# Optimization experiments

Hardware: AMD Instinct MI355X
Metric: run time of the kernel (lower is better)

## Reference

```python
import jax, jax.numpy as jnp
import numpy as np

N, E = 50000, 800000
IN_D, HID_D, OUT_D = 128, 128, 64
BN_EPS = 1e-5


def setup_inputs() -> dict:
    key = jax.random.key(0)
    ks = jax.random.split(key, 16)
    x = jax.random.normal(ks[0], (N, IN_D), dtype=jnp.float32)
    edge_index = jax.random.randint(ks[1], (2, E), 0, N, dtype=jnp.int64)
    edge_weight = jax.random.uniform(ks[2], (E,), dtype=jnp.float32)
    s = 0.05  # xavier-ish small gain
    inp = {
        'x': x, 'edge_index': edge_index, 'edge_weight': edge_weight,
        # SAGEConv 1: lin_l (aggregated, with bias), lin_r (root, no bias)
        'W1l': jax.random.normal(ks[3], (HID_D, IN_D), jnp.float32) * s,
        'b1': jnp.zeros((HID_D,), jnp.float32),
        'W1r': jax.random.normal(ks[4], (HID_D, IN_D), jnp.float32) * s,
        # SAGEConv 2
        'W2l': jax.random.normal(ks[5], (HID_D, HID_D), jnp.float32) * s,
        'b2': jnp.zeros((HID_D,), jnp.float32),
        'W2r': jax.random.normal(ks[6], (HID_D, HID_D), jnp.float32) * s,
        # SAGEConv 3
        'W3l': jax.random.normal(ks[7], (OUT_D, HID_D), jnp.float32) * s,
        'b3': jnp.zeros((OUT_D,), jnp.float32),
        'W3r': jax.random.normal(ks[8], (OUT_D, HID_D), jnp.float32) * s,
        # BatchNorm (eval mode: running stats)
        'bn1_g': jnp.ones((HID_D,), jnp.float32),
        'bn1_b': jnp.zeros((HID_D,), jnp.float32),
        'bn1_m': jax.random.normal(ks[9], (HID_D,), jnp.float32) * 0.01,
        'bn1_v': jnp.ones((HID_D,), jnp.float32) + jax.random.uniform(ks[10], (HID_D,), jnp.float32) * 0.1,
        'bn2_g': jnp.ones((HID_D,), jnp.float32),
        'bn2_b': jnp.zeros((HID_D,), jnp.float32),
        'bn2_m': jax.random.normal(ks[11], (HID_D,), jnp.float32) * 0.01,
        'bn2_v': jnp.ones((HID_D,), jnp.float32) + jax.random.uniform(ks[12], (HID_D,), jnp.float32) * 0.1,
    }
    return inp


def _sage_conv(x, src, dst, ew, Wl, bl, Wr):
    # message: x_j * w_ij ; aggregate: mean over incoming edges of node i
    msg = x[src] * ew[:, None]                      # [E, D]
    agg = jax.ops.segment_sum(msg, dst, num_segments=N)
    cnt = jax.ops.segment_sum(jnp.ones_like(ew), dst, num_segments=N)
    mean = agg / jnp.maximum(cnt, 1.0)[:, None]     # [N, D]
    return mean @ Wl.T + bl + x @ Wr.T


def _bn_eval(x, g, b, m, v):
    return (x - m) * (g * jax.lax.rsqrt(v + BN_EPS)) + b


def reference(x, edge_index, edge_weight,
              W1l, b1, W1r, W2l, b2, W2r, W3l, b3, W3r,
              bn1_g, bn1_b, bn1_m, bn1_v, bn2_g, bn2_b, bn2_m, bn2_v):
    src, dst = edge_index[0], edge_index[1]
    h = _sage_conv(x, src, dst, edge_weight, W1l, b1, W1r)
    h = _bn_eval(h, bn1_g, bn1_b, bn1_m, bn1_v)
    h = jnp.where(h >= 0, h, 0.1 * h)  # leaky_relu(0.1); dropout inactive (eval)
    h = _sage_conv(h, src, dst, edge_weight, W2l, b2, W2r)
    h = _bn_eval(h, bn2_g, bn2_b, bn2_m, bn2_v)
    h = jnp.where(h >= 0, h, 0.1 * h)
    h = _sage_conv(h, src, dst, edge_weight, W3l, b3, W3r)
    # F.normalize(p=2, dim=1)
    norm = jnp.maximum(jnp.linalg.norm(h, axis=1, keepdims=True), 1e-12)
    return h / norm
```

## Files before the change

kernel.cpp:

```cpp
#include <hip/hip_runtime.h>
#include <hip/hip_bf16.h>

#define IN_D 128
#define BN_EPS 1e-5f

typedef short bf8 __attribute__((ext_vector_type(8)));
typedef float f32x4 __attribute__((ext_vector_type(4)));

__device__ __forceinline__ ushort f2bf(float f) {
    unsigned u = __float_as_uint(f);
    unsigned r = u + 0x7fffu + ((u >> 16) & 1u);
    return (ushort)(r >> 16);
}


__global__ void k_hist(const int* __restrict__ ei, int* __restrict__ deg, int E, int n) {
    int e = blockIdx.x * 256 + threadIdx.x;
    if (e < E) {
        int dst = ei[E + e];
        if (dst >= 0 && dst < n) atomicAdd(&deg[dst], 1);
    }
}

__global__ void k_block_sum(const int* __restrict__ deg, int* __restrict__ bsum, int n) {
    __shared__ int sdata[256];
    int i = blockIdx.x * 256 + threadIdx.x;
    int v = (i < n) ? deg[i] : 0;
    sdata[threadIdx.x] = v;
    __syncthreads();
    for (int s = 128; s > 0; s >>= 1) {
        if (threadIdx.x < s) sdata[threadIdx.x] += sdata[threadIdx.x + s];
        __syncthreads();
    }
    if (threadIdx.x == 0) bsum[blockIdx.x] = sdata[0];
}

__global__ void k_scan_bsum(int* __restrict__ bsum, int nb) {
    __shared__ int s[256];
    int t = threadIdx.x;
    int v = (t < nb) ? bsum[t] : 0;
    s[t] = v;
    __syncthreads();
    for (int off = 1; off < 256; off <<= 1) {
        int u = (t >= off) ? s[t - off] : 0;
        __syncthreads();
        s[t] += u;
        __syncthreads();
    }
    if (t < nb) bsum[t] = s[t] - v;
}

__global__ void k_scan_deg(const int* __restrict__ deg, const int* __restrict__ boff,
                           int* __restrict__ rowptr, int* __restrict__ cursor,
                           float* __restrict__ invcnt, int n) {
    __shared__ int s[256];
    int t = threadIdx.x;
    int i = blockIdx.x * 256 + t;
    int v = (i < n) ? deg[i] : 0;
    s[t] = v;
    __syncthreads();
    for (int off = 1; off < 256; off <<= 1) {
        int u = (t >= off) ? s[t - off] : 0;
        __syncthreads();
        s[t] += u;
        __syncthreads();
    }
    int incl = s[t];
    int excl = incl - v;
    int base = boff[blockIdx.x];
    if (i < n) {
        rowptr[i] = base + excl;
        cursor[i] = base + excl;
        invcnt[i] = 1.0f / (float)(v < 1 ? 1 : v);
        if (i == n - 1) rowptr[n] = base + incl;
    }
}

__global__ void k_fill(const int* __restrict__ ei, const float* __restrict__ ew,
                       int* __restrict__ cursor, int2* __restrict__ csr, int E, int n) {
    int e = blockIdx.x * 256 + threadIdx.x;
    if (e < E) {
        int dst = ei[E + e];
        int src = ei[e];
        if (dst < 0 || dst >= n) return;
        if (src < 0) src = 0;
        if (src >= n) src = n - 1;
        int slot = atomicAdd(&cursor[dst], 1);
        int2 p;
        p.x = src;
        p.y = __float_as_int(ew[e]);
        csr[slot] = p;
    }
}

__global__ void k_cvt(const float4* __restrict__ X4, ushort4* __restrict__ Ob, int n4) {
    int i = blockIdx.x * 256 + threadIdx.x;
    if (i < n4) {
        float4 f = X4[i];
        ushort4 o;
        o.x = f2bf(f.x); o.y = f2bf(f.y); o.z = f2bf(f.z); o.w = f2bf(f.w);
        Ob[i] = o;
    }
}

__global__ void k_prep(const float* __restrict__ W1l, const float* __restrict__ W1r,
                       const float* __restrict__ W2l, const float* __restrict__ W2r,
                       const float* __restrict__ W3l, const float* __restrict__ W3r,
                       ushort* __restrict__ WB1, ushort* __restrict__ WB2,
                       ushort* __restrict__ WB3) {
    int e = blockIdx.x * 256 + threadIdx.x;
    const float *Wl, *Wr;
    ushort* dst;
    int idx;
    if (e < 32768)      { Wl = W1l; Wr = W1r; dst = WB1; idx = e; }
    else if (e < 65536) { Wl = W2l; Wr = W2r; dst = WB2; idx = e - 32768; }
    else                { Wl = W3l; Wr = W3r; dst = WB3; idx = e - 65536; }
    int ei = idx & 7, j0 = (idx >> 3) & 15, g = (idx >> 7) & 3, kc = (idx >> 9) & 7,
        jc = idx >> 12;
    int ksrc = (kc & 3) * 32 + g * 8 + ei;
    int jsrc = jc * 16 + j0;
    const float* src = (kc < 4) ? Wl : Wr;
    dst[idx] = f2bf(src[jsrc * 128 + ksrc]);
}

__global__ void k_agg(const unsigned* __restrict__ Xb2, const int* __restrict__ rowptr,
                      const int2* __restrict__ csr, const float* __restrict__ invcnt,
                      unsigned* __restrict__ Mb2, int n) {
    int wid = (blockIdx.x * blockDim.x + threadIdx.x) >> 6;
    int lane = threadIdx.x & 63;
    if (wid >= n) return;
    int beg = __builtin_amdgcn_readfirstlane(rowptr[wid]);
    int end = __builtin_amdgcn_readfirstlane(rowptr[wid + 1]);
    float ax = 0.f, ay = 0.f;
    int k = beg;
    for (; k + 4 <= end; k += 4) {
        int2 e0 = csr[k], e1 = csr[k + 1], e2 = csr[k + 2], e3 = csr[k + 3];
        unsigned v0 = Xb2[(size_t)e0.x * 64 + lane];
        unsigned v1 = Xb2[(size_t)e1.x * 64 + lane];
        unsigned v2 = Xb2[(size_t)e2.x * 64 + lane];
        unsigned v3 = Xb2[(size_t)e3.x * 64 + lane];
        float w0 = __int_as_float(e0.y), w1 = __int_as_float(e1.y);
        float w2 = __int_as_float(e2.y), w3 = __int_as_float(e3.y);
        ax += w0 * __uint_as_float(v0 << 16) + w1 * __uint_as_float(v1 << 16) +
              w2 * __uint_as_float(v2 << 16) + w3 * __uint_as_float(v3 << 16);
        ay += w0 * __uint_as_float(v0 & 0xffff0000u) + w1 * __uint_as_float(v1 & 0xffff0000u) +
              w2 * __uint_as_float(v2 & 0xffff0000u) + w3 * __uint_as_float(v3 & 0xffff0000u);
    }
    for (; k < end; ++k) {
        int2 e = csr[k];
        float w = __int_as_float(e.y);
        unsigned v = Xb2[(size_t)e.x * 64 + lane];
        ax += w * __uint_as_float(v << 16);
        ay += w * __uint_as_float(v & 0xffff0000u);
    }
    float ic = invcnt[wid];
    Mb2[(size_t)wid * 64 + lane] =
        (unsigned)f2bf(ax * ic) | ((unsigned)f2bf(ay * ic) << 16);
}

template <int DO, int BN_FLAG>
__global__ __launch_bounds__(256) void k_gemm5(
    const ushort* __restrict__ Mb, const ushort* __restrict__ Xb,
    const ushort* __restrict__ WB, const float* __restrict__ bias,
    const float* __restrict__ bng, const float* __restrict__ bnb,
    const float* __restrict__ bnm, const float* __restrict__ bnv,
    void* __restrict__ OutP, int n) {
    constexpr int CF = DO / 64;
    __shared__ ushort sAb[32 * 256];
    __shared__ float ssrow[32];

    int t = threadIdx.x;
    int wv = t >> 6;
    int lane = t & 63;
    int rowl = lane & 15;
    int g = lane >> 4;
    int node0 = blockIdx.x * 32;

    {
        const uint4* Ms = (const uint4*)(Mb + (size_t)node0 * 128);
        const uint4* Xs = (const uint4*)(Xb + (size_t)node0 * 128);
        uint4 z = make_uint4(0, 0, 0, 0);
#pragma unroll
        for (int it = 0; it < 4; ++it) {
            int idx = it * 256 + t;
            int nd = idx >> 5;
            int u = idx & 31;
            bool ok = (node0 + nd) < n;
            uint4 vv = ok ? (u < 16 ? Ms[nd * 16 + u] : Xs[nd * 16 + (u - 16)]) : z;
            int byte = nd * 512 + ((u * 16) ^ ((nd & 7) << 4));
            *(uint4*)((char*)sAb + byte) = vv;
        }
        if (BN_FLAG == 0 && t < 32) ssrow[t] = 0.f;
    }
    __syncthreads();

    f32x4 acc[2][CF];
#pragma unroll
    for (int nf = 0; nf < 2; ++nf)
#pragma unroll
        for (int cf = 0; cf < CF; ++cf) acc[nf][cf] = (f32x4)0.f;

#pragma unroll
    for (int kc = 0; kc < 8; ++kc) {
        bf8 a[2];
#pragma unroll
        for (int nf = 0; nf < 2; ++nf) {
            int nl = nf * 16 + rowl;
            int byte = nl * 512 + (((kc * 64) + g * 16) ^ ((nl & 7) << 4));
            a[nf] = *(const bf8*)((const char*)sAb + byte);
        }
#pragma unroll
        for (int cf = 0; cf < CF; ++cf) {
            int jc = wv * CF + cf;
            bf8 b = *(const bf8*)(WB + (((jc * 8 + kc) * 4 + g) * 128 + rowl * 8));
#pragma unroll
            for (int nf = 0; nf < 2; ++nf)
                acc[nf][cf] =
                    __builtin_amdgcn_mfma_f32_16x16x32_bf16(a[nf], b, acc[nf][cf], 0, 0, 0);
        }
    }

    if constexpr (BN_FLAG) {
        __syncthreads();
        ushort* sH = sAb;
#pragma unroll
        for (int cf = 0; cf < CF; ++cf) {
            int j = (wv * CF + cf) * 16 + rowl;
            float bj = bias[j];
            float gm = bng[j], bb = bnb[j], mm = bnm[j];
            float iv = rsqrtf(bnv[j] + BN_EPS);
#pragma unroll
            for (int nf = 0; nf < 2; ++nf) {
#pragma unroll
                for (int r = 0; r < 4; ++r) {
                    int nrow = nf * 16 + g * 4 + r;
                    float h = acc[nf][cf][r] + bj;
                    h = (h - mm) * (gm * iv) + bb;
                    h = h >= 0.f ? h : 0.1f * h;
                    sH[nrow * DO + j] = f2bf(h);
                }
            }
        }
        __syncthreads();
        ushort* Hout = (ushort*)OutP;
        constexpr int UPR = DO / 8;
#pragma unroll
        for (int it = 0; it < (32 * UPR) / 256; ++it) {
            int u = it * 256 + t;
            int nd = u / UPR, c = u % UPR;
            if (node0 + nd < n)
                *(uint4*)(Hout + (size_t)(node0 + nd) * DO + c * 8) =
                    *(uint4*)&sH[nd * DO + c * 8];
        }
    } else {
        float* Outf = (float*)OutP;
        int j = wv * 16 + rowl;
        float bj = bias[j];
        float h[2][4];
#pragma unroll
        for (int nf = 0; nf < 2; ++nf)
#pragma unroll
            for (int r = 0; r < 4; ++r) {
                h[nf][r] = acc[nf][0][r] + bj;
                float s = h[nf][r] * h[nf][r];
                s += __shfl_xor(s, 1);
                s += __shfl_xor(s, 2);
                s += __shfl_xor(s, 4);
                s += __shfl_xor(s, 8);
                if (rowl == 0) atomicAdd(&ssrow[nf * 16 + g * 4 + r], s);
            }
        __syncthreads();
#pragma unroll
        for (int nf = 0; nf < 2; ++nf)
#pragma unroll
            for (int r = 0; r < 4; ++r) {
                int nrow = nf * 16 + g * 4 + r;
                int node = node0 + nrow;
                if (node < n) {
                    float sc = 1.0f / fmaxf(sqrtf(ssrow[nrow]), 1e-12f);
                    Outf[(size_t)node * 64 + j] = h[nf][r] * sc;
                }
            }
    }
}


extern "C" void kernel_launch(void* const* d_in, const int* in_sizes, int n_in,
                              void* d_out, int out_size, void* d_ws, size_t ws_size,
                              hipStream_t stream) {
    const float* x = (const float*)d_in[0];
    const int* ei = (const int*)d_in[1];
    const float* ew = (const float*)d_in[2];
    const float* W1l = (const float*)d_in[3];
    const float* b1 = (const float*)d_in[4];
    const float* W1r = (const float*)d_in[5];
    const float* W2l = (const float*)d_in[6];
    const float* b2 = (const float*)d_in[7];
    const float* W2r = (const float*)d_in[8];
    const float* W3l = (const float*)d_in[9];
    const float* b3 = (const float*)d_in[10];
    const float* W3r = (const float*)d_in[11];
    const float* bn1_g = (const float*)d_in[12];
    const float* bn1_b = (const float*)d_in[13];
    const float* bn1_m = (const float*)d_in[14];
    const float* bn1_v = (const float*)d_in[15];
    const float* bn2_g = (const float*)d_in[16];
    const float* bn2_b = (const float*)d_in[17];
    const float* bn2_m = (const float*)d_in[18];
    const float* bn2_v = (const float*)d_in[19];

    const int N = in_sizes[0] / IN_D;
    const int E = in_sizes[2];
    float* out = (float*)d_out;

    char* p = (char*)d_ws;
    auto alloc = [&](size_t bytes) -> void* {
        void* r = (void*)p;
        p += (bytes + 255) & ~(size_t)255;
        return r;
    };
    int* deg = (int*)alloc((size_t)N * 4);
    int* rowptr = (int*)alloc((size_t)(N + 1) * 4);
    int* cursor = (int*)alloc((size_t)N * 4);
    float* invcnt = (float*)alloc((size_t)N * 4);
    int* bsum = (int*)alloc(256 * 4);
    int2* csr = (int2*)alloc((size_t)E * 8);
    ushort* xb = (ushort*)alloc((size_t)N * 128 * 2);
    ushort* Mb = (ushort*)alloc((size_t)N * 128 * 2);
    ushort* H1b = (ushort*)alloc((size_t)N * 128 * 2);
    ushort* H2b = (ushort*)alloc((size_t)N * 128 * 2);
    ushort* WB1 = (ushort*)alloc(32768 * 2);
    ushort* WB2 = (ushort*)alloc(32768 * 2);
    ushort* WB3 = (ushort*)alloc(16384 * 2);

    const int NB = (N + 255) / 256;
    const int EB = (E + 255) / 256;
    const int AGG_B = (N + 3) / 4;
    const int GEMM_B = (N + 31) / 32;
    const int CVT_B = (N * 128 / 4 + 255) / 256;

    hipMemsetAsync(deg, 0, (size_t)N * 4, stream);
    k_hist<<<EB, 256, 0, stream>>>(ei, deg, E, N);
    k_prep<<<320, 256, 0, stream>>>(W1l, W1r, W2l, W2r, W3l, W3r, WB1, WB2, WB3);
    k_cvt<<<CVT_B, 256, 0, stream>>>((const float4*)x, (ushort4*)xb, N * 128 / 4);
    k_block_sum<<<NB, 256, 0, stream>>>(deg, bsum, N);
    k_scan_bsum<<<1, 256, 0, stream>>>(bsum, NB);
    k_scan_deg<<<NB, 256, 0, stream>>>(deg, bsum, rowptr, cursor, invcnt, N);
    k_fill<<<EB, 256, 0, stream>>>(ei, ew, cursor, csr, E, N);

    k_agg<<<AGG_B, 256, 0, stream>>>((const unsigned*)xb, rowptr, csr, invcnt,
                                     (unsigned*)Mb, N);
    k_gemm5<128, 1><<<GEMM_B, 256, 0, stream>>>(Mb, xb, WB1, b1, bn1_g, bn1_b, bn1_m,
                                                bn1_v, (void*)H1b, N);
    k_agg<<<AGG_B, 256, 0, stream>>>((const unsigned*)H1b, rowptr, csr, invcnt,
                                     (unsigned*)Mb, N);
    k_gemm5<128, 1><<<GEMM_B, 256, 0, stream>>>(Mb, H1b, WB2, b2, bn2_g, bn2_b, bn2_m,
                                                bn2_v, (void*)H2b, N);
    k_agg<<<AGG_B, 256, 0, stream>>>((const unsigned*)H2b, rowptr, csr, invcnt,
                                     (unsigned*)Mb, N);
    k_gemm5<64, 0><<<GEMM_B, 256, 0, stream>>>(Mb, H2b, WB3, b3, nullptr, nullptr,
                                               nullptr, nullptr, (void*)out, N);
}
```

Before: 341.5 us.

## Pack CSR entries to 32 bits and gather two edges per wave

Each CSR entry becomes a single 32-bit word: a 16-bit source index and a bf16 edge weight, replacing the int2 pair. The aggregation kernel now splits each wave into two halves. Each half processes a different edge and loads 8 bytes per lane, and the halves are combined with a cross-half shuffle before the write. This halves CSR traffic and doubles edges in flight per wave to reduce gather latency. The cost is rounding edge weights to bf16 and a 16-bit source index that only works while N stays below 65536.

```diff
diff --git a/kernel.cpp b/kernel.cpp
--- a/kernel.cpp
+++ b/kernel.cpp
@@ -77,7 +77,8 @@
 }
 
 __global__ void k_fill(const int* __restrict__ ei, const float* __restrict__ ew,
-                       int* __restrict__ cursor, int2* __restrict__ csr, int E, int n) {
+                       int* __restrict__ cursor, unsigned* __restrict__ csr, int E,
+                       int n) {
     int e = blockIdx.x * 256 + threadIdx.x;
     if (e < E) {
         int dst = ei[E + e];
@@ -86,10 +87,7 @@
         if (src < 0) src = 0;
         if (src >= n) src = n - 1;
         int slot = atomicAdd(&cursor[dst], 1);
-        int2 p;
-        p.x = src;
-        p.y = __float_as_int(ew[e]);
-        csr[slot] = p;
+        csr[slot] = (unsigned)(src & 0xffff) | ((unsigned)f2bf(ew[e]) << 16);
     }
 }
 
@@ -123,39 +121,42 @@
     dst[idx] = f2bf(src[jsrc * 128 + ksrc]);
 }
 
-__global__ void k_agg(const unsigned* __restrict__ Xb2, const int* __restrict__ rowptr,
-                      const int2* __restrict__ csr, const float* __restrict__ invcnt,
-                      unsigned* __restrict__ Mb2, int n) {
+__global__ void k_agg(const uint2* __restrict__ X4, const int* __restrict__ rowptr,
+                      const unsigned* __restrict__ csr, const float* __restrict__ invcnt,
+                      uint2* __restrict__ M4, int n) {
     int wid = (blockIdx.x * blockDim.x + threadIdx.x) >> 6;
     int lane = threadIdx.x & 63;
     if (wid >= n) return;
     int beg = __builtin_amdgcn_readfirstlane(rowptr[wid]);
     int end = __builtin_amdgcn_readfirstlane(rowptr[wid + 1]);
-    float ax = 0.f, ay = 0.f;
-    int k = beg;
-    for (; k + 4 <= end; k += 4) {
-        int2 e0 = csr[k], e1 = csr[k + 1], e2 = csr[k + 2], e3 = csr[k + 3];
-        unsigned v0 = Xb2[(size_t)e0.x * 64 + lane];
-        unsigned v1 = Xb2[(size_t)e1.x * 64 + lane];
-        unsigned v2 = Xb2[(size_t)e2.x * 64 + lane];
-        unsigned v3 = Xb2[(size_t)e3.x * 64 + lane];
-        float w0 = __int_as_float(e0.y), w1 = __int_as_float(e1.y);
-        float w2 = __int_as_float(e2.y), w3 = __int_as_float(e3.y);
-        ax += w0 * __uint_as_float(v0 << 16) + w1 * __uint_as_float(v1 << 16) +
-              w2 * __uint_as_float(v2 << 16) + w3 * __uint_as_float(v3 << 16);
-        ay += w0 * __uint_as_float(v0 & 0xffff0000u) + w1 * __uint_as_float(v1 & 0xffff0000u) +
-              w2 * __uint_as_float(v2 & 0xffff0000u) + w3 * __uint_as_float(v3 & 0xffff0000u);
-    }
-    for (; k < end; ++k) {
-        int2 e = csr[k];
-        float w = __int_as_float(e.y);
-        unsigned v = Xb2[(size_t)e.x * 64 + lane];
-        ax += w * __uint_as_float(v << 16);
-        ay += w * __uint_as_float(v & 0xffff0000u);
-    }
-    float ic = invcnt[wid];
-    Mb2[(size_t)wid * 64 + lane] =
-        (unsigned)f2bf(ax * ic) | ((unsigned)f2bf(ay * ic) << 16);
+    int half = lane >> 5;
+    int dl = lane & 31;
+    float a0 = 0.f, a1 = 0.f, a2 = 0.f, a3 = 0.f;
+    for (int k = beg; k < end; k += 8) {
+#pragma unroll
+        for (int u = 0; u < 4; ++u) {
+            int kk = k + u * 2 + half;
+            unsigned e = (kk < end) ? csr[kk] : 0u;
+            float w = __uint_as_float(e & 0xffff0000u);
+            int src = e & 0xffff;
+            uint2 v = X4[(size_t)src * 32 + dl];
+            a0 += w * __uint_as_float(v.x << 16);
+            a1 += w * __uint_as_float(v.x & 0xffff0000u);
+            a2 += w * __uint_as_float(v.y << 16);
+            a3 += w * __uint_as_float(v.y & 0xffff0000u);
+        }
+    }
+    a0 += __shfl_xor(a0, 32);
+    a1 += __shfl_xor(a1, 32);
+    a2 += __shfl_xor(a2, 32);
+    a3 += __shfl_xor(a3, 32);
+    if (half == 0) {
+        float ic = invcnt[wid];
+        uint2 o;
+        o.x = (unsigned)f2bf(a0 * ic) | ((unsigned)f2bf(a1 * ic) << 16);
+        o.y = (unsigned)f2bf(a2 * ic) | ((unsigned)f2bf(a3 * ic) << 16);
+        M4[(size_t)wid * 32 + dl] = o;
+    }
 }
 
 template <int DO, int BN_FLAG>
@@ -324,7 +325,7 @@
     int* cursor = (int*)alloc((size_t)N * 4);
     float* invcnt = (float*)alloc((size_t)N * 4);
     int* bsum = (int*)alloc(256 * 4);
-    int2* csr = (int2*)alloc((size_t)E * 8);
+    unsigned* csr = (unsigned*)alloc((size_t)(E + 16) * 4);
     ushort* xb = (ushort*)alloc((size_t)N * 128 * 2);
     ushort* Mb = (ushort*)alloc((size_t)N * 128 * 2);
     ushort* H1b = (ushort*)alloc((size_t)N * 128 * 2);
@@ -348,16 +349,16 @@
     k_scan_deg<<<NB, 256, 0, stream>>>(deg, bsum, rowptr, cursor, invcnt, N);
     k_fill<<<EB, 256, 0, stream>>>(ei, ew, cursor, csr, E, N);
 
-    k_agg<<<AGG_B, 256, 0, stream>>>((const unsigned*)xb, rowptr, csr, invcnt,
-                                     (unsigned*)Mb, N);
+    k_agg<<<AGG_B, 256, 0, stream>>>((const uint2*)xb, rowptr, csr, invcnt,
+                                     (uint2*)Mb, N);
     k_gemm5<128, 1><<<GEMM_B, 256, 0, stream>>>(Mb, xb, WB1, b1, bn1_g, bn1_b, bn1_m,
                                                 bn1_v, (void*)H1b, N);
-    k_agg<<<AGG_B, 256, 0, stream>>>((const unsigned*)H1b, rowptr, csr, invcnt,
-                                     (unsigned*)Mb, N);
+    k_agg<<<AGG_B, 256, 0, stream>>>((const uint2*)H1b, rowptr, csr, invcnt,
+                                     (uint2*)Mb, N);
     k_gemm5<128, 1><<<GEMM_B, 256, 0, stream>>>(Mb, H1b, WB2, b2, bn2_g, bn2_b, bn2_m,
                                                 bn2_v, (void*)H2b, N);
-    k_agg<<<AGG_B, 256, 0, stream>>>((const unsigned*)H2b, rowptr, csr, invcnt,
-                                     (unsigned*)Mb, N);
+    k_agg<<<AGG_B, 256, 0, stream>>>((const uint2*)H2b, rowptr, csr, invcnt,
+                                     (uint2*)Mb, N);
     k_gemm5<64, 0><<<GEMM_B, 256, 0, stream>>>(Mb, H2b, WB3, b3, nullptr, nullptr,
                                                nullptr, nullptr, (void*)out, N);
 }
```

Result: slower. 369.3 us (+8.2%).
